# Kernel tuning notes

Hardware: AMD Instinct MI355X
Metric: run time of the kernel (lower is better)

## Reference

```python
import jax, jax.numpy as jnp
import numpy as np

N, E, G = 100000, 500000, 1000


def _gat(h_in, src, dst, W, a_s, a_d, b, n):
    # PyG GATConv, heads=1, concat=True, negative_slope=0.2, self-loops already in src/dst
    h = h_in @ W.T                                  # [N, out]
    alpha_src = h @ a_s                             # [N]
    alpha_dst = h @ a_d                             # [N]
    e = jax.nn.leaky_relu(alpha_src[src] + alpha_dst[dst], 0.2)  # [E']
    m = jax.ops.segment_max(e, dst, num_segments=n)
    ex = jnp.exp(e - m[dst])
    den = jax.ops.segment_sum(ex, dst, num_segments=n)
    alpha = ex / den[dst]                           # segment softmax over incoming edges
    out = jax.ops.segment_sum(h[src] * alpha[:, None], dst, num_segments=n)
    return out + b


def _forward(x, edge_index, batch, w1, b1, w2, b2, w3, b3,
             g1w, g1as, g1ad, g1b, g2w, g2as, g2ad, g2b,
             g3w, g3as, g3ad, g3b, g4w, g4as, g4ad, g4b,
             g5w, g5as, g5ad, g5b, lw, lb):
    n = x.shape[0]
    h = jax.nn.relu(x @ w1.T + b1)
    h = jax.nn.relu(h @ w2.T + b2)
    h = jax.nn.relu(h @ w3.T + b3)
    loops = jnp.arange(n)
    src = jnp.concatenate([edge_index[0], loops])   # add self-loops
    dst = jnp.concatenate([edge_index[1], loops])
    h = jax.nn.relu(_gat(h, src, dst, g1w, g1as, g1ad, g1b, n))
    h = jax.nn.relu(_gat(h, src, dst, g2w, g2as, g2ad, g2b, n))
    h = jax.nn.relu(_gat(h, src, dst, g3w, g3as, g3ad, g3b, n))
    h = jax.nn.relu(_gat(h, src, dst, g4w, g4as, g4ad, g4b, n))
    h = jax.nn.relu(_gat(h, src, dst, g5w, g5as, g5ad, g5b, n))
    sums = jax.ops.segment_sum(h, batch, num_segments=G)            # [G,32]
    cnt = jax.ops.segment_sum(jnp.ones((n,), h.dtype), batch, num_segments=G)
    mean = sums / jnp.maximum(cnt, 1.0)[:, None]
    return jax.nn.sigmoid(mean @ lw.T + lb)         # [G,1]


def setup_inputs() -> dict:
    key = jax.random.key(0)
    ks = jax.random.split(key, 24)

    def lin(k, o, i):
        k1, k2 = jax.random.split(k)
        s = 1.0 / np.sqrt(i)
        return (jax.random.uniform(k1, (o, i), jnp.float32, -s, s),
                jax.random.uniform(k2, (o,), jnp.float32, -s, s))

    def gat_p(k, i, o):
        k1, k2, k3 = jax.random.split(k, 3)
        s = 1.0 / np.sqrt(i)
        W = jax.random.uniform(k1, (o, i), jnp.float32, -s, s)
        a_s = jax.random.normal(k2, (o,), jnp.float32) / np.sqrt(o)
        a_d = jax.random.normal(k3, (o,), jnp.float32) / np.sqrt(o)
        return W, a_s, a_d, jnp.zeros((o,), jnp.float32)

    inp = {}
    inp['x'] = jax.random.normal(ks[0], (N, 1), jnp.float32)
    inp['edge_index'] = jax.random.randint(ks[1], (2, E), 0, N)
    inp['batch'] = jnp.sort(jax.random.randint(ks[2], (N,), 0, G))
    inp['w1'], inp['b1'] = lin(ks[3], 16, 1)
    inp['w2'], inp['b2'] = lin(ks[4], 32, 16)
    inp['w3'], inp['b3'] = lin(ks[5], 64, 32)
    dims = [(64, 128), (128, 256), (256, 128), (128, 64), (64, 32)]
    for j, (i, o) in enumerate(dims, start=1):
        W, a_s, a_d, b = gat_p(ks[5 + j], i, o)
        inp[f'g{j}w'], inp[f'g{j}as'], inp[f'g{j}ad'], inp[f'g{j}b'] = W, a_s, a_d, b
    inp['lw'], inp['lb'] = lin(ks[12], 1, 32)
    return inp


def reference(x, edge_index, batch, w1, b1, w2, b2, w3, b3,
              g1w, g1as, g1ad, g1b, g2w, g2as, g2ad, g2b,
              g3w, g3as, g3ad, g3b, g4w, g4as, g4ad, g4b,
              g5w, g5as, g5ad, g5b, lw, lb):
    return _forward(x, edge_index, batch, w1, b1, w2, b2, w3, b3,
                    g1w, g1as, g1ad, g1b, g2w, g2as, g2ad, g2b,
                    g3w, g3as, g3ad, g3b, g4w, g4as, g4ad, g4b,
                    g5w, g5as, g5ad, g5b, lw, lb)
```

## Files before the change

### kernel.cpp

```cpp
#include <hip/hip_runtime.h>
#include <math.h>

typedef __attribute__((ext_vector_type(8))) __bf16 bf16x8;
typedef __attribute__((ext_vector_type(4))) float f32x4;

__device__ inline unsigned short f2bf(float f) {
    unsigned int i = __float_as_uint(f);
    unsigned int r = i + 0x7fffu + ((i >> 16) & 1u);
    return (unsigned short)(r >> 16);
}
__device__ inline float bf2f(unsigned short u) {
    return __uint_as_float(((unsigned int)u) << 16);
}

__global__ __launch_bounds__(256) void prelude_kernel(
    const float* __restrict__ x,
    const float* __restrict__ w1, const float* __restrict__ b1,
    const float* __restrict__ w2, const float* __restrict__ b2,
    const float* __restrict__ w3, const float* __restrict__ b3,
    unsigned short* __restrict__ h0, int n,
    const float* __restrict__ g0, const float* __restrict__ g1, const float* __restrict__ g2,
    const float* __restrict__ g3, const float* __restrict__ g4,
    unsigned short* __restrict__ wbAll,
    const int* __restrict__ batch, int* __restrict__ gstart, int G,
    const int* __restrict__ dst, int* __restrict__ deg, int E,
    int mlpB, int f2bfB, int gsB) {
    int b = blockIdx.x;
    int tid = threadIdx.x;
    if (b < mlpB) {
        __shared__ float sw1[16], sb1[16], sw2[32 * 16], sb2[32], sw3[64 * 32], sb3[64];
        if (tid < 16) { sw1[tid] = w1[tid]; sb1[tid] = b1[tid]; }
        if (tid < 32) sb2[tid] = b2[tid];
        if (tid < 64) sb3[tid] = b3[tid];
        for (int i = tid; i < 512; i += 256) sw2[i] = w2[i];
        for (int i = tid; i < 2048; i += 256) sw3[i] = w3[i];
        __syncthreads();
        int node = b * 256 + tid;
        if (node >= n) return;
        float xv = x[node];
        float t1[16], t2[32];
#pragma unroll
        for (int i = 0; i < 16; i++) t1[i] = fmaxf(sw1[i] * xv + sb1[i], 0.f);
#pragma unroll
        for (int o = 0; o < 32; o++) {
            float a = sb2[o];
#pragma unroll
            for (int i = 0; i < 16; i++) a += sw2[o * 16 + i] * t1[i];
            t2[o] = fmaxf(a, 0.f);
        }
        uint4* gp = (uint4*)(h0 + (size_t)node * 64);
#pragma unroll
        for (int c = 0; c < 8; c++) {
            unsigned int wvec[4];
#pragma unroll
            for (int p = 0; p < 4; p++) {
                int o = c * 8 + p * 2;
                float a0 = sb3[o], a1 = sb3[o + 1];
#pragma unroll
                for (int i = 0; i < 32; i++) {
                    a0 += sw3[o * 32 + i] * t2[i];
                    a1 += sw3[(o + 1) * 32 + i] * t2[i];
                }
                wvec[p] =
                    (unsigned)f2bf(fmaxf(a0, 0.f)) | ((unsigned)f2bf(fmaxf(a1, 0.f)) << 16);
            }
            gp[c] = make_uint4(wvec[0], wvec[1], wvec[2], wvec[3]);
        }
    } else if (b < mlpB + f2bfB) {
        int i = (b - mlpB) * 256 + tid;
        float v;
        if (i < 8192) v = g0[i];
        else if (i < 40960) v = g1[i - 8192];
        else if (i < 73728) v = g2[i - 40960];
        else if (i < 81920) v = g3[i - 73728];
        else if (i < 83968) v = g4[i - 81920];
        else return;
        wbAll[i] = f2bf(v);
    } else if (b < mlpB + f2bfB + gsB) {
        int g = (b - mlpB - f2bfB) * 256 + tid;
        if (g > G) return;
        if (g == G) { gstart[G] = n; return; }
        int lo = 0, hi = n;
        while (lo < hi) {
            int mid = (lo + hi) >> 1;
            if (batch[mid] < g) lo = mid + 1;
            else hi = mid;
        }
        gstart[g] = lo;
    } else {
        int e = (b - mlpB - f2bfB - gsB) * 256 + tid;
        if (e >= E + n) return;
        int d = (e < E) ? dst[e] : (e - E);
        atomicAdd(&deg[d], 1);
    }
}

template <int BN>
__global__ __launch_bounds__(256) void gemm_mfma(
    const unsigned short* __restrict__ A, const unsigned short* __restrict__ Wb,
    unsigned short* __restrict__ Cb,
    const float* __restrict__ avs, const float* __restrict__ avd,
    float* __restrict__ as_, float* __restrict__ ad_, int n, int K, int O) {
    constexpr int SN = BN / 32;
    __shared__ unsigned short As[128][72];
    __shared__ unsigned short Ws[BN][72];
    int tid = threadIdx.x;
    int row0 = blockIdx.x * 128, col0 = blockIdx.y * BN;
    int w = tid >> 6, lane = tid & 63;
    int wr = w >> 1, wc = w & 1;
    int quad = lane >> 4, l15 = lane & 15;
    f32x4 acc[4][SN];
#pragma unroll
    for (int mi = 0; mi < 4; mi++)
#pragma unroll
        for (int ni = 0; ni < SN; ni++) acc[mi][ni] = (f32x4){0.f, 0.f, 0.f, 0.f};

    for (int k0 = 0; k0 < K; k0 += 64) {
#pragma unroll
        for (int i = tid; i < 1024; i += 256) {
            int r = i >> 3, c8 = i & 7;
            int gr = row0 + r;
            uint4 v = make_uint4(0u, 0u, 0u, 0u);
            if (gr < n) v = *(const uint4*)(A + (size_t)gr * K + k0 + c8 * 8);
            *(uint4*)&As[r][c8 * 8] = v;
        }
#pragma unroll
        for (int i = tid; i < BN * 8; i += 256) {
            int r = i >> 3, c8 = i & 7;
            uint4 v = *(const uint4*)(Wb + (size_t)(col0 + r) * K + k0 + c8 * 8);
            *(uint4*)&Ws[r][c8 * 8] = v;
        }
        __syncthreads();
#pragma unroll
        for (int kk = 0; kk < 64; kk += 32) {
            bf16x8 bfr[SN];
#pragma unroll
            for (int ni = 0; ni < SN; ni++)
                bfr[ni] = *(const bf16x8*)&Ws[wc * (BN / 2) + ni * 16 + l15][kk + quad * 8];
#pragma unroll
            for (int mi = 0; mi < 4; mi++) {
                bf16x8 afr = *(const bf16x8*)&As[wr * 64 + mi * 16 + l15][kk + quad * 8];
#pragma unroll
                for (int ni = 0; ni < SN; ni++)
                    acc[mi][ni] = __builtin_amdgcn_mfma_f32_16x16x32_bf16(afr, bfr[ni],
                                                                          acc[mi][ni], 0, 0, 0);
            }
        }
        __syncthreads();
    }
    float avsv[SN], avdv[SN];
    int gc[SN];
#pragma unroll
    for (int ni = 0; ni < SN; ni++) {
        gc[ni] = col0 + wc * (BN / 2) + ni * 16 + l15;
        avsv[ni] = avs[gc[ni]];
        avdv[ni] = avd[gc[ni]];
    }
#pragma unroll
    for (int mi = 0; mi < 4; mi++) {
        int gm0 = row0 + wr * 64 + mi * 16 + quad * 4;
        float ps[4] = {0.f, 0.f, 0.f, 0.f}, pd[4] = {0.f, 0.f, 0.f, 0.f};
#pragma unroll
        for (int ni = 0; ni < SN; ni++) {
#pragma unroll
            for (int r = 0; r < 4; r++) {
                float d = acc[mi][ni][r];
                int gm = gm0 + r;
                if (gm < n) Cb[(size_t)gm * O + gc[ni]] = f2bf(d);
                ps[r] += d * avsv[ni];
                pd[r] += d * avdv[ni];
            }
        }
#pragma unroll
        for (int r = 0; r < 4; r++) {
#pragma unroll
            for (int m = 1; m <= 8; m <<= 1) {
                ps[r] += __shfl_xor(ps[r], m);
                pd[r] += __shfl_xor(pd[r], m);
            }
        }
        if (l15 == 0) {
#pragma unroll
            for (int r = 0; r < 4; r++) {
                int gm = gm0 + r;
                if (gm < n) {
                    atomicAdd(&as_[gm], ps[r]);
                    atomicAdd(&ad_[gm], pd[r]);
                }
            }
        }
    }
}

__global__ void scan_block_sums(const int* __restrict__ deg, int* __restrict__ bsums, int n) {
    __shared__ int sdata[256];
    int tid = threadIdx.x;
    int base = blockIdx.x * 1024 + tid * 4;
    int s = 0;
    for (int i = 0; i < 4; i++) {
        int g = base + i;
        if (g < n) s += deg[g];
    }
    sdata[tid] = s;
    __syncthreads();
    for (int off = 128; off > 0; off >>= 1) {
        if (tid < off) sdata[tid] += sdata[tid + off];
        __syncthreads();
    }
    if (tid == 0) bsums[blockIdx.x] = sdata[0];
}

__global__ void scan_write(const int* __restrict__ deg, const int* __restrict__ bsums,
                           int* __restrict__ rowptr, int* __restrict__ cursor, int n, int nb) {
    __shared__ int sdata[256];
    int tid = threadIdx.x;
    sdata[tid] = (tid < blockIdx.x && tid < nb) ? bsums[tid] : 0;
    __syncthreads();
    for (int off = 128; off > 0; off >>= 1) {
        if (tid < off) sdata[tid] += sdata[tid + off];
        __syncthreads();
    }
    int base = sdata[0];
    __syncthreads();
    int gbase = blockIdx.x * 1024 + tid * 4;
    int v[4];
    int s = 0;
    for (int i = 0; i < 4; i++) {
        int g = gbase + i;
        v[i] = (g < n) ? deg[g] : 0;
        s += v[i];
    }
    sdata[tid] = s;
    __syncthreads();
    for (int off = 1; off < 256; off <<= 1) {
        int t = (tid >= off) ? sdata[tid - off] : 0;
        __syncthreads();
        sdata[tid] += t;
        __syncthreads();
    }
    int excl = sdata[tid] - s + base;
    for (int i = 0; i < 4; i++) {
        int g = gbase + i;
        if (g < n) { rowptr[g] = excl; cursor[g] = excl; }
        excl += v[i];
    }
    if (blockIdx.x == gridDim.x - 1 && tid == 255) rowptr[n] = base + sdata[255];
}

__global__ void scatter_kernel(const int* __restrict__ esrc_in, const int* __restrict__ edst_in,
                               int* __restrict__ cursor, int* __restrict__ esrc, int E, int n) {
    int e = blockIdx.x * 256 + threadIdx.x;
    if (e >= E + n) return;
    int s, d;
    if (e < E) { s = esrc_in[e]; d = edst_in[e]; }
    else { s = e - E; d = e - E; }
    int pos = atomicAdd(&cursor[d], 1);
    esrc[pos] = s;
}

template <int O>
__global__ __launch_bounds__(256) void gat_aggregate(
    const unsigned short* __restrict__ hl, const float* __restrict__ as_,
    const float* __restrict__ ad_, const int* __restrict__ rowptr,
    const int* __restrict__ esrc, const float* __restrict__ bias,
    unsigned short* __restrict__ hout, int n, float* __restrict__ zeroBuf, int zeroCnt) {
    int gtid = blockIdx.x * 256 + threadIdx.x;
    if (gtid < zeroCnt) zeroBuf[gtid] = 0.f;
    constexpr int C8 = O / 8;
    constexpr int EPW = 64 / C8;
    int v = blockIdx.x * 4 + (threadIdx.x >> 6);
    int lane = threadIdx.x & 63;
    if (v >= n) return;
    int beg = rowptr[v], end = rowptr[v + 1];
    int deg = end - beg;
    float adv = ad_[v];
    int sub = lane / C8;
    int c = lane % C8;
    float acc[8] = {0.f, 0.f, 0.f, 0.f, 0.f, 0.f, 0.f, 0.f};
    if (deg <= 64) {
        int sreg = v;
        float e = -1e30f;
        if (lane < deg) {
            sreg = esrc[beg + lane];
            float t = as_[sreg] + adv;
            e = (t > 0.f) ? t : 0.2f * t;
        }
        float m = e;
#pragma unroll
        for (int o = 32; o > 0; o >>= 1) m = fmaxf(m, __shfl_xor(m, o));
        float ex = (lane < deg) ? __expf(e - m) : 0.f;
        float sum = ex;
#pragma unroll
        for (int o = 32; o > 0; o >>= 1) sum += __shfl_xor(sum, o);
        float alpha_r = ex / sum;
        for (int j0 = 0; j0 < deg; j0 += EPW) {
            int idx = j0 + sub;
            int cidx = (idx < deg) ? idx : 0;
            float alpha = __shfl(alpha_r, cidx);
            int s2 = __shfl(sreg, cidx);
            if (idx >= deg) alpha = 0.f;
            uint4 raw = ((const uint4*)(hl + (size_t)s2 * O))[c];
            acc[0] += alpha * __uint_as_float(raw.x << 16);
            acc[1] += alpha * __uint_as_float(raw.x & 0xffff0000u);
            acc[2] += alpha * __uint_as_float(raw.y << 16);
            acc[3] += alpha * __uint_as_float(raw.y & 0xffff0000u);
            acc[4] += alpha * __uint_as_float(raw.z << 16);
            acc[5] += alpha * __uint_as_float(raw.z & 0xffff0000u);
            acc[6] += alpha * __uint_as_float(raw.w << 16);
            acc[7] += alpha * __uint_as_float(raw.w & 0xffff0000u);
        }
    } else {
        float mymax = -1e30f;
        for (int j = beg + lane; j < end; j += 64) {
            float e = as_[esrc[j]] + adv;
            e = (e > 0.f) ? e : 0.2f * e;
            mymax = fmaxf(mymax, e);
        }
#pragma unroll
        for (int o = 32; o > 0; o >>= 1) mymax = fmaxf(mymax, __shfl_xor(mymax, o));
        float mysum = 0.f;
        for (int j = beg + lane; j < end; j += 64) {
            float e = as_[esrc[j]] + adv;
            e = (e > 0.f) ? e : 0.2f * e;
            mysum += __expf(e - mymax);
        }
#pragma unroll
        for (int o = 32; o > 0; o >>= 1) mysum += __shfl_xor(mysum, o);
        float invden = 1.f / mysum;
        for (int j0 = beg; j0 < end; j0 += EPW) {
            int j = j0 + sub;
            bool valid = j < end;
            int s = valid ? esrc[j] : v;
            float e = as_[s] + adv;
            e = (e > 0.f) ? e : 0.2f * e;
            float alpha = valid ? __expf(e - mymax) * invden : 0.f;
            uint4 raw = ((const uint4*)(hl + (size_t)s * O))[c];
            acc[0] += alpha * __uint_as_float(raw.x << 16);
            acc[1] += alpha * __uint_as_float(raw.x & 0xffff0000u);
            acc[2] += alpha * __uint_as_float(raw.y << 16);
            acc[3] += alpha * __uint_as_float(raw.y & 0xffff0000u);
            acc[4] += alpha * __uint_as_float(raw.z << 16);
            acc[5] += alpha * __uint_as_float(raw.z & 0xffff0000u);
            acc[6] += alpha * __uint_as_float(raw.w << 16);
            acc[7] += alpha * __uint_as_float(raw.w & 0xffff0000u);
        }
    }
#pragma unroll
    for (int o = C8; o < 64; o <<= 1)
#pragma unroll
        for (int k = 0; k < 8; k++) acc[k] += __shfl_xor(acc[k], o);
    if (sub == 0) {
        unsigned short ov[8];
#pragma unroll
        for (int k = 0; k < 8; k++) ov[k] = f2bf(fmaxf(acc[k] + bias[c * 8 + k], 0.f));
        uint4 packed;
        packed.x = (unsigned)ov[0] | ((unsigned)ov[1] << 16);
        packed.y = (unsigned)ov[2] | ((unsigned)ov[3] << 16);
        packed.z = (unsigned)ov[4] | ((unsigned)ov[5] << 16);
        packed.w = (unsigned)ov[6] | ((unsigned)ov[7] << 16);
        ((uint4*)(hout + (size_t)v * O))[c] = packed;
    }
}

__global__ __launch_bounds__(256) void pool_final_kernel(
    const unsigned short* __restrict__ h, const int* __restrict__ start,
    const float* __restrict__ lw, const float* __restrict__ lb,
    float* __restrict__ out, int G) {
    __shared__ float red[8][33];
    int g = blockIdx.x;
    if (g >= G) return;
    int beg = start[g], end = start[g + 1];
    int tid = threadIdx.x;
    int nodeLane = tid >> 5, f = tid & 31;
    float acc = 0.f;
    for (int v = beg + nodeLane; v < end; v += 8)
        acc += bf2f(h[(size_t)v * 32 + f]);
    red[nodeLane][f] = acc;
    __syncthreads();
    if (tid < 32) {
        float s = 0.f;
#pragma unroll
        for (int i = 0; i < 8; i++) s += red[i][f];
        float inv = 1.f / fmaxf((float)(end - beg), 1.f);
        float val = s * inv * lw[f];
#pragma unroll
        for (int o = 16; o > 0; o >>= 1) val += __shfl_xor(val, o);
        if (f == 0) out[g] = 1.f / (1.f + __expf(-(val + lb[0])));
    }
}

extern "C" void kernel_launch(void* const* d_in, const int* in_sizes, int n_in,
                              void* d_out, int out_size, void* d_ws, size_t ws_size,
                              hipStream_t stream) {
    const float* x = (const float*)d_in[0];
    const int* ei = (const int*)d_in[1];
    const int* batch = (const int*)d_in[2];
    const float* w1 = (const float*)d_in[3];
    const float* b1 = (const float*)d_in[4];
    const float* w2 = (const float*)d_in[5];
    const float* b2 = (const float*)d_in[6];
    const float* w3 = (const float*)d_in[7];
    const float* b3 = (const float*)d_in[8];
    const float* gw[5];
    const float* gas[5];
    const float* gad[5];
    const float* gb[5];
    for (int l = 0; l < 5; l++) {
        gw[l] = (const float*)d_in[9 + l * 4 + 0];
        gas[l] = (const float*)d_in[9 + l * 4 + 1];
        gad[l] = (const float*)d_in[9 + l * 4 + 2];
        gb[l] = (const float*)d_in[9 + l * 4 + 3];
    }
    const float* lw = (const float*)d_in[29];
    const float* lb = (const float*)d_in[30];
    float* out = (float*)d_out;

    int N = in_sizes[0];
    int E = in_sizes[1] / 2;
    int G = out_size;
    int Etot = E + N;

    char* ws = (char*)d_ws;
    size_t off = 0;
    auto alloc = [&](size_t bytes) -> void* {
        void* p = ws + off;
        off = (off + bytes + 255) & ~(size_t)255;
        return p;
    };
    unsigned short* actA = (unsigned short*)alloc((size_t)N * 256 * 2);
    unsigned short* actB = (unsigned short*)alloc((size_t)N * 256 * 2);
    char* zblock = (char*)alloc((size_t)N * 20);
    float* asad0 = (float*)zblock;
    float* asad1 = asad0 + (size_t)N * 2;
    int* deg = (int*)(zblock + (size_t)N * 16);
    int* rowptr = (int*)alloc((size_t)(N + 1) * 4);
    int* cursor = (int*)alloc((size_t)(N + 1) * 4);
    int* esrc = (int*)alloc((size_t)Etot * 4);
    int* bsums = (int*)alloc(4096);
    int* gstart = (int*)alloc((size_t)(G + 1) * 4);
    unsigned short* wbAll = (unsigned short*)alloc((size_t)83968 * 2);
    const int woff[5] = {0, 8192, 40960, 73728, 81920};
    unsigned short* wb[5];
    for (int l = 0; l < 5; l++) wb[l] = wbAll + woff[l];
    (void)ws_size;
    (void)n_in;

    hipMemsetAsync(zblock, 0, (size_t)N * 20, stream);

    int mlpB = (N + 255) / 256;
    int f2bfB = (83968 + 255) / 256;
    int gsB = (G + 1 + 255) / 256;
    int histB = (Etot + 255) / 256;
    prelude_kernel<<<mlpB + f2bfB + gsB + histB, 256, 0, stream>>>(
        x, w1, b1, w2, b2, w3, b3, actA, N, gw[0], gw[1], gw[2], gw[3], gw[4], wbAll, batch,
        gstart, G, ei + E, deg, E, mlpB, f2bfB, gsB);

    int nb = (N + 1023) / 1024;
    scan_block_sums<<<nb, 256, 0, stream>>>(deg, bsums, N);
    scan_write<<<nb, 256, 0, stream>>>(deg, bsums, rowptr, cursor, N, nb);
    scatter_kernel<<<(Etot + 255) / 256, 256, 0, stream>>>(ei, ei + E, cursor, esrc, E, N);

    const int Ks[5] = {64, 128, 256, 128, 64};
    const int Os[5] = {128, 256, 128, 64, 32};
    int aggBlocks = (N + 3) / 4;
    int gx = (N + 127) / 128;
    for (int l = 0; l < 5; l++) {
        int K = Ks[l], O = Os[l];
        float* asb = (l & 1) ? asad1 : asad0;
        float* zbuf = (l & 1) ? asad0 : asad1;
        if (O >= 64) {
            dim3 grid(gx, O / 64);
            gemm_mfma<64><<<grid, 256, 0, stream>>>(actA, wb[l], actB, gas[l], gad[l], asb,
                                                    asb + N, N, K, O);
        } else {
            dim3 grid(gx, 1);
            gemm_mfma<32><<<grid, 256, 0, stream>>>(actA, wb[l], actB, gas[l], gad[l], asb,
                                                    asb + N, N, K, O);
        }
        switch (O) {
            case 256:
                gat_aggregate<256><<<aggBlocks, 256, 0, stream>>>(
                    actB, asb, asb + N, rowptr, esrc, gb[l], actA, N, zbuf, 2 * N);
                break;
            case 128:
                gat_aggregate<128><<<aggBlocks, 256, 0, stream>>>(
                    actB, asb, asb + N, rowptr, esrc, gb[l], actA, N, zbuf, 2 * N);
                break;
            case 64:
                gat_aggregate<64><<<aggBlocks, 256, 0, stream>>>(
                    actB, asb, asb + N, rowptr, esrc, gb[l], actA, N, zbuf, 2 * N);
                break;
            default:
                gat_aggregate<32><<<aggBlocks, 256, 0, stream>>>(
                    actB, asb, asb + N, rowptr, esrc, gb[l], actA, N, zbuf, 2 * N);
                break;
        }
    }

    pool_final_kernel<<<G, 256, 0, stream>>>(actA, gstart, lw, lb, out, G);
}
```

Before: 573.9 us.

## Precompute W^T·a attention vectors and compute alpha from GEMM input tile

Folds the attention projections into per-layer vectors u_s = W^T a_s and u_d = W^T a_d, computed once in the prelude. Alpha_src and alpha_dst are now taken as dot products of the input rows with u inside the col0==0 GEMM block and written directly, replacing the per-block shuffle reductions and float atomics. This also removes the zeroing of alpha buffers inside the aggregation kernel and shrinks the memset. The prelude MLP is restructured so 8 threads share one node, each computing 8 outputs with a transposed W3 in shared memory. Alpha is now computed from bf16 inputs and fp32 u rather than fp32 GEMM outputs, so rounding changes slightly.

```diff
diff --git a/kernel.cpp b/kernel.cpp
--- a/kernel.cpp
+++ b/kernel.cpp
@@ -12,6 +12,9 @@
 __device__ inline float bf2f(unsigned short u) {
     return __uint_as_float(((unsigned int)u) << 16);
 }
+
+#define F2BF_B 329
+#define U_B 3
 
 __global__ __launch_bounds__(256) void prelude_kernel(
     const float* __restrict__ x,
@@ -22,20 +25,28 @@
     const float* __restrict__ g0, const float* __restrict__ g1, const float* __restrict__ g2,
     const float* __restrict__ g3, const float* __restrict__ g4,
     unsigned short* __restrict__ wbAll,
+    const float* __restrict__ s0, const float* __restrict__ s1, const float* __restrict__ s2,
+    const float* __restrict__ s3, const float* __restrict__ s4,
+    const float* __restrict__ d0, const float* __restrict__ d1, const float* __restrict__ d2,
+    const float* __restrict__ d3, const float* __restrict__ d4,
+    float* __restrict__ uAll,
     const int* __restrict__ batch, int* __restrict__ gstart, int G,
     const int* __restrict__ dst, int* __restrict__ deg, int E,
-    int mlpB, int f2bfB, int gsB) {
+    int mlpB, int gsB) {
     int b = blockIdx.x;
     int tid = threadIdx.x;
     if (b < mlpB) {
-        __shared__ float sw1[16], sb1[16], sw2[32 * 16], sb2[32], sw3[64 * 32], sb3[64];
+        __shared__ float sw1[16], sb1[16], sw2[512], sb2[32], sw3t[2048], sb3[64];
         if (tid < 16) { sw1[tid] = w1[tid]; sb1[tid] = b1[tid]; }
         if (tid < 32) sb2[tid] = b2[tid];
         if (tid < 64) sb3[tid] = b3[tid];
         for (int i = tid; i < 512; i += 256) sw2[i] = w2[i];
-        for (int i = tid; i < 2048; i += 256) sw3[i] = w3[i];
-        __syncthreads();
-        int node = b * 256 + tid;
+        for (int i = tid; i < 2048; i += 256) {
+            int ii = i >> 6, o = i & 63;
+            sw3t[i] = w3[o * 32 + ii];
+        }
+        __syncthreads();
+        int node = b * 32 + (tid >> 3), oct = tid & 7;
         if (node >= n) return;
         float xv = x[node];
         float t1[16], t2[32];
@@ -48,25 +59,22 @@
             for (int i = 0; i < 16; i++) a += sw2[o * 16 + i] * t1[i];
             t2[o] = fmaxf(a, 0.f);
         }
-        uint4* gp = (uint4*)(h0 + (size_t)node * 64);
-#pragma unroll
-        for (int c = 0; c < 8; c++) {
-            unsigned int wvec[4];
-#pragma unroll
-            for (int p = 0; p < 4; p++) {
-                int o = c * 8 + p * 2;
-                float a0 = sb3[o], a1 = sb3[o + 1];
-#pragma unroll
-                for (int i = 0; i < 32; i++) {
-                    a0 += sw3[o * 32 + i] * t2[i];
-                    a1 += sw3[(o + 1) * 32 + i] * t2[i];
-                }
-                wvec[p] =
-                    (unsigned)f2bf(fmaxf(a0, 0.f)) | ((unsigned)f2bf(fmaxf(a1, 0.f)) << 16);
-            }
-            gp[c] = make_uint4(wvec[0], wvec[1], wvec[2], wvec[3]);
-        }
-    } else if (b < mlpB + f2bfB) {
+        float av[8];
+#pragma unroll
+        for (int j = 0; j < 8; j++) av[j] = sb3[oct * 8 + j];
+#pragma unroll
+        for (int i = 0; i < 32; i++) {
+            float t = t2[i];
+#pragma unroll
+            for (int j = 0; j < 8; j++) av[j] += sw3t[i * 64 + oct * 8 + j] * t;
+        }
+        unsigned int wv[4];
+#pragma unroll
+        for (int p = 0; p < 4; p++)
+            wv[p] = (unsigned)f2bf(fmaxf(av[2 * p], 0.f)) |
+                    ((unsigned)f2bf(fmaxf(av[2 * p + 1], 0.f)) << 16);
+        ((uint4*)(h0 + (size_t)node * 64 + oct * 8))[0] = make_uint4(wv[0], wv[1], wv[2], wv[3]);
+    } else if (b < mlpB + F2BF_B) {
         int i = (b - mlpB) * 256 + tid;
         float v;
         if (i < 8192) v = g0[i];
@@ -76,8 +84,8 @@
         else if (i < 83968) v = g4[i - 81920];
         else return;
         wbAll[i] = f2bf(v);
-    } else if (b < mlpB + f2bfB + gsB) {
-        int g = (b - mlpB - f2bfB) * 256 + tid;
+    } else if (b < mlpB + F2BF_B + gsB) {
+        int g = (b - mlpB - F2BF_B) * 256 + tid;
         if (g > G) return;
         if (g == G) { gstart[G] = n; return; }
         int lo = 0, hi = n;
@@ -87,8 +95,29 @@
             else hi = mid;
         }
         gstart[g] = lo;
+    } else if (b < mlpB + F2BF_B + gsB + U_B) {
+        int idx = (b - mlpB - F2BF_B - gsB) * 256 + tid;
+        if (idx >= 640) return;
+        int l, st, K, O;
+        if (idx < 64) { l = 0; st = 0; K = 64; O = 128; }
+        else if (idx < 192) { l = 1; st = 64; K = 128; O = 256; }
+        else if (idx < 448) { l = 2; st = 192; K = 256; O = 128; }
+        else if (idx < 576) { l = 3; st = 448; K = 128; O = 64; }
+        else { l = 4; st = 576; K = 64; O = 32; }
+        const float* W = (l == 0) ? g0 : (l == 1) ? g1 : (l == 2) ? g2 : (l == 3) ? g3 : g4;
+        const float* as = (l == 0) ? s0 : (l == 1) ? s1 : (l == 2) ? s2 : (l == 3) ? s3 : s4;
+        const float* ad = (l == 0) ? d0 : (l == 1) ? d1 : (l == 2) ? d2 : (l == 3) ? d3 : d4;
+        int k = idx - st;
+        float us = 0.f, ud = 0.f;
+        for (int o = 0; o < O; o++) {
+            float w = W[o * K + k];
+            us += w * as[o];
+            ud += w * ad[o];
+        }
+        uAll[idx] = us;
+        uAll[640 + idx] = ud;
     } else {
-        int e = (b - mlpB - f2bfB - gsB) * 256 + tid;
+        int e = (b - mlpB - F2BF_B - gsB - U_B) * 256 + tid;
         if (e >= E + n) return;
         int d = (e < E) ? dst[e] : (e - E);
         atomicAdd(&deg[d], 1);
@@ -99,7 +128,7 @@
 __global__ __launch_bounds__(256) void gemm_mfma(
     const unsigned short* __restrict__ A, const unsigned short* __restrict__ Wb,
     unsigned short* __restrict__ Cb,
-    const float* __restrict__ avs, const float* __restrict__ avd,
+    const float* __restrict__ us, const float* __restrict__ ud,
     float* __restrict__ as_, float* __restrict__ ad_, int n, int K, int O) {
     constexpr int SN = BN / 32;
     __shared__ unsigned short As[128][72];
@@ -114,6 +143,8 @@
     for (int mi = 0; mi < 4; mi++)
 #pragma unroll
         for (int ni = 0; ni < SN; ni++) acc[mi][ni] = (f32x4){0.f, 0.f, 0.f, 0.f};
+    float uacc_s = 0.f, uacc_d = 0.f;
+    int urow = tid & 127, uhalf = tid >> 7;
 
     for (int k0 = 0; k0 < K; k0 += 64) {
 #pragma unroll
@@ -131,6 +162,20 @@
             *(uint4*)&Ws[r][c8 * 8] = v;
         }
         __syncthreads();
+        if (col0 == 0) {
+            int kb = uhalf * 32;
+#pragma unroll
+            for (int q = 0; q < 8; q++) {
+                uint2 rawv = *(const uint2*)&As[urow][kb + q * 4];
+                float a0 = __uint_as_float(rawv.x << 16);
+                float a1 = __uint_as_float(rawv.x & 0xffff0000u);
+                float a2 = __uint_as_float(rawv.y << 16);
+                float a3 = __uint_as_float(rawv.y & 0xffff0000u);
+                int kk = k0 + kb + q * 4;
+                uacc_s += a0 * us[kk] + a1 * us[kk + 1] + a2 * us[kk + 2] + a3 * us[kk + 3];
+                uacc_d += a0 * ud[kk] + a1 * ud[kk + 1] + a2 * ud[kk + 2] + a3 * ud[kk + 3];
+            }
+        }
 #pragma unroll
         for (int kk = 0; kk < 64; kk += 32) {
             bf16x8 bfr[SN];
@@ -148,45 +193,31 @@
         }
         __syncthreads();
     }
-    float avsv[SN], avdv[SN];
+    if (col0 == 0) {
+        float* red = (float*)&As[0][0];
+        red[tid] = uacc_s;
+        red[256 + tid] = uacc_d;
+        __syncthreads();
+        if (tid < 128) {
+            int gr = row0 + tid;
+            if (gr < n) {
+                as_[gr] = red[tid] + red[tid + 128];
+                ad_[gr] = red[256 + tid] + red[384 + tid];
+            }
+        }
+    }
     int gc[SN];
 #pragma unroll
-    for (int ni = 0; ni < SN; ni++) {
-        gc[ni] = col0 + wc * (BN / 2) + ni * 16 + l15;
-        avsv[ni] = avs[gc[ni]];
-        avdv[ni] = avd[gc[ni]];
-    }
+    for (int ni = 0; ni < SN; ni++) gc[ni] = col0 + wc * (BN / 2) + ni * 16 + l15;
 #pragma unroll
     for (int mi = 0; mi < 4; mi++) {
         int gm0 = row0 + wr * 64 + mi * 16 + quad * 4;
-        float ps[4] = {0.f, 0.f, 0.f, 0.f}, pd[4] = {0.f, 0.f, 0.f, 0.f};
 #pragma unroll
         for (int ni = 0; ni < SN; ni++) {
-#pragma unroll
-            for (int r = 0; r < 4; r++) {
-                float d = acc[mi][ni][r];
-                int gm = gm0 + r;
-                if (gm < n) Cb[(size_t)gm * O + gc[ni]] = f2bf(d);
-                ps[r] += d * avsv[ni];
-                pd[r] += d * avdv[ni];
-            }
-        }
-#pragma unroll
-        for (int r = 0; r < 4; r++) {
-#pragma unroll
-            for (int m = 1; m <= 8; m <<= 1) {
-                ps[r] += __shfl_xor(ps[r], m);
-                pd[r] += __shfl_xor(pd[r], m);
-            }
-        }
-        if (l15 == 0) {
 #pragma unroll
             for (int r = 0; r < 4; r++) {
                 int gm = gm0 + r;
-                if (gm < n) {
-                    atomicAdd(&as_[gm], ps[r]);
-                    atomicAdd(&ad_[gm], pd[r]);
-                }
+                if (gm < n) Cb[(size_t)gm * O + gc[ni]] = f2bf(acc[mi][ni][r]);
             }
         }
     }
@@ -263,9 +294,7 @@
     const unsigned short* __restrict__ hl, const float* __restrict__ as_,
     const float* __restrict__ ad_, const int* __restrict__ rowptr,
     const int* __restrict__ esrc, const float* __restrict__ bias,
-    unsigned short* __restrict__ hout, int n, float* __restrict__ zeroBuf, int zeroCnt) {
-    int gtid = blockIdx.x * 256 + threadIdx.x;
-    if (gtid < zeroCnt) zeroBuf[gtid] = 0.f;
+    unsigned short* __restrict__ hout, int n) {
     constexpr int C8 = O / 8;
     constexpr int EPW = 64 / C8;
     int v = blockIdx.x * 4 + (threadIdx.x >> 6);
@@ -429,31 +458,32 @@
     };
     unsigned short* actA = (unsigned short*)alloc((size_t)N * 256 * 2);
     unsigned short* actB = (unsigned short*)alloc((size_t)N * 256 * 2);
-    char* zblock = (char*)alloc((size_t)N * 20);
-    float* asad0 = (float*)zblock;
-    float* asad1 = asad0 + (size_t)N * 2;
-    int* deg = (int*)(zblock + (size_t)N * 16);
+    float* asb = (float*)alloc((size_t)N * 8);
+    float* adb = asb + N;
+    int* deg = (int*)alloc((size_t)N * 4);
     int* rowptr = (int*)alloc((size_t)(N + 1) * 4);
     int* cursor = (int*)alloc((size_t)(N + 1) * 4);
     int* esrc = (int*)alloc((size_t)Etot * 4);
     int* bsums = (int*)alloc(4096);
     int* gstart = (int*)alloc((size_t)(G + 1) * 4);
     unsigned short* wbAll = (unsigned short*)alloc((size_t)83968 * 2);
+    float* uAll = (float*)alloc((size_t)1280 * 4);
     const int woff[5] = {0, 8192, 40960, 73728, 81920};
+    const int uoff[5] = {0, 64, 192, 448, 576};
     unsigned short* wb[5];
     for (int l = 0; l < 5; l++) wb[l] = wbAll + woff[l];
     (void)ws_size;
     (void)n_in;
 
-    hipMemsetAsync(zblock, 0, (size_t)N * 20, stream);
-
-    int mlpB = (N + 255) / 256;
-    int f2bfB = (83968 + 255) / 256;
+    hipMemsetAsync(deg, 0, (size_t)N * 4, stream);
+
+    int mlpB = (N + 31) / 32;
     int gsB = (G + 1 + 255) / 256;
     int histB = (Etot + 255) / 256;
-    prelude_kernel<<<mlpB + f2bfB + gsB + histB, 256, 0, stream>>>(
-        x, w1, b1, w2, b2, w3, b3, actA, N, gw[0], gw[1], gw[2], gw[3], gw[4], wbAll, batch,
-        gstart, G, ei + E, deg, E, mlpB, f2bfB, gsB);
+    prelude_kernel<<<mlpB + F2BF_B + gsB + U_B + histB, 256, 0, stream>>>(
+        x, w1, b1, w2, b2, w3, b3, actA, N, gw[0], gw[1], gw[2], gw[3], gw[4], wbAll,
+        gas[0], gas[1], gas[2], gas[3], gas[4], gad[0], gad[1], gad[2], gad[3], gad[4], uAll,
+        batch, gstart, G, ei + E, deg, E, mlpB, gsB);
 
     int nb = (N + 1023) / 1024;
     scan_block_sums<<<nb, 256, 0, stream>>>(deg, bsums, N);
@@ -466,33 +496,31 @@
     int gx = (N + 127) / 128;
     for (int l = 0; l < 5; l++) {
         int K = Ks[l], O = Os[l];
-        float* asb = (l & 1) ? asad1 : asad0;
-        float* zbuf = (l & 1) ? asad0 : asad1;
+        const float* us = uAll + uoff[l];
+        const float* ud = uAll + 640 + uoff[l];
         if (O >= 64) {
             dim3 grid(gx, O / 64);
-            gemm_mfma<64><<<grid, 256, 0, stream>>>(actA, wb[l], actB, gas[l], gad[l], asb,
-                                                    asb + N, N, K, O);
+            gemm_mfma<64><<<grid, 256, 0, stream>>>(actA, wb[l], actB, us, ud, asb, adb, N, K, O);
         } else {
             dim3 grid(gx, 1);
-            gemm_mfma<32><<<grid, 256, 0, stream>>>(actA, wb[l], actB, gas[l], gad[l], asb,
-                                                    asb + N, N, K, O);
+            gemm_mfma<32><<<grid, 256, 0, stream>>>(actA, wb[l], actB, us, ud, asb, adb, N, K, O);
         }
         switch (O) {
             case 256:
-                gat_aggregate<256><<<aggBlocks, 256, 0, stream>>>(
-                    actB, asb, asb + N, rowptr, esrc, gb[l], actA, N, zbuf, 2 * N);
+                gat_aggregate<256><<<aggBlocks, 256, 0, stream>>>(actB, asb, adb, rowptr, esrc,
+                                                                  gb[l], actA, N);
                 break;
             case 128:
-                gat_aggregate<128><<<aggBlocks, 256, 0, stream>>>(
-                    actB, asb, asb + N, rowptr, esrc, gb[l], actA, N, zbuf, 2 * N);
+                gat_aggregate<128><<<aggBlocks, 256, 0, stream>>>(actB, asb, adb, rowptr, esrc,
+                                                                  gb[l], actA, N);
                 break;
             case 64:
-                gat_aggregate<64><<<aggBlocks, 256, 0, stream>>>(
-                    actB, asb, asb + N, rowptr, esrc, gb[l], actA, N, zbuf, 2 * N);
+                gat_aggregate<64><<<aggBlocks, 256, 0, stream>>>(actB, asb, adb, rowptr, esrc,
+                                                                 gb[l], actA, N);
                 break;
             default:
-                gat_aggregate<32><<<aggBlocks, 256, 0, stream>>>(
-                    actB, asb, asb + N, rowptr, esrc, gb[l], actA, N, zbuf, 2 * N);
+                gat_aggregate<32><<<aggBlocks, 256, 0, stream>>>(actB, asb, adb, rowptr, esrc,
+                                                                 gb[l], actA, N);
                 break;
         }
     }
```

New measurement: 653.8 us. 1.14x slower.
